# Performance work log

Measured on AMD Instinct MI355X. Metric: run time of the kernel, lower is better.

## Reference

```python
import jax, jax.numpy as jnp
import numpy as np

LN_EPS = 1e-5

def _layernorm(x, g, b):
    mu = jnp.mean(x, axis=-1, keepdims=True)
    var = jnp.mean(jnp.square(x - mu), axis=-1, keepdims=True)
    return (x - mu) * jax.lax.rsqrt(var + LN_EPS) * g + b

def setup_inputs() -> dict:
    key = jax.random.key(0)
    ks = jax.random.split(key, 12)
    B, S, E = 8, 4096, 512
    H, DK = 64, 8          # d_k = E // H = 8 qubits per head
    NQ_FFN, FFN = 8, 2048
    TWO_PI = 2.0 * np.pi
    x = jax.random.normal(ks[0], (B, S, E), dtype=jnp.float32)
    # trainable RX phases per attention head/wire; trainable RY phases for FFN qubits
    theta_attn = jax.random.uniform(ks[1], (H, DK), dtype=jnp.float32, maxval=TWO_PI)
    theta_ffn = jax.random.uniform(ks[2], (NQ_FFN,), dtype=jnp.float32, maxval=TWO_PI)
    s_e = 1.0 / np.sqrt(E)
    W_comb = jax.random.uniform(ks[3], (E, E), dtype=jnp.float32, minval=-s_e, maxval=s_e)
    b_comb = jax.random.uniform(ks[4], (E,), dtype=jnp.float32, minval=-s_e, maxval=s_e)
    s_q = 1.0 / np.sqrt(NQ_FFN)
    W1 = jax.random.uniform(ks[5], (FFN, NQ_FFN), dtype=jnp.float32, minval=-s_q, maxval=s_q)
    b1 = jax.random.uniform(ks[6], (FFN,), dtype=jnp.float32, minval=-s_q, maxval=s_q)
    s_f = 1.0 / np.sqrt(FFN)
    W2 = jax.random.uniform(ks[7], (E, FFN), dtype=jnp.float32, minval=-s_f, maxval=s_f)
    b2 = jax.random.uniform(ks[8], (E,), dtype=jnp.float32, minval=-s_f, maxval=s_f)
    ln1_g = jnp.ones((E,), jnp.float32); ln1_b = jnp.zeros((E,), jnp.float32)
    ln2_g = jnp.ones((E,), jnp.float32); ln2_b = jnp.zeros((E,), jnp.float32)
    return {"x": x, "theta_attn": theta_attn, "W_comb": W_comb, "b_comb": b_comb,
            "ln1_g": ln1_g, "ln1_b": ln1_b, "theta_ffn": theta_ffn,
            "W1": W1, "b1": b1, "W2": W2, "b2": b2, "ln2_g": ln2_g, "ln2_b": ln2_b}

def reference(x, theta_attn, W_comb, b_comb, ln1_g, ln1_b, theta_ffn, W1, b1, W2, b2, ln2_g, ln2_b):
    B, S, E = x.shape
    H, DK = theta_attn.shape
    NQ = theta_ffn.shape[0]
    # Quantum attention heads: RX(x) then RX(theta) on |0> per wire -> <Z> = cos(x+theta)
    q = jnp.cos(x.reshape(B, S, H, DK) + theta_attn)  # [B,S,H,DK]
    attn_out = jnp.einsum('bse,fe->bsf', q.reshape(B, S, E), W_comb) + b_comb
    x1 = _layernorm(x + attn_out, ln1_g, ln1_b)
    # Quantum FFN layer: RY(x) then RY(theta) -> <Z> = cos(x+theta), first NQ features only
    fq = jnp.cos(x1[..., :NQ] + theta_ffn)            # [B,S,NQ]
    h = jax.nn.relu(jnp.einsum('bsq,fq->bsf', fq, W1) + b1)
    ffn_out = jnp.einsum('bsf,ef->bse', h, W2) + b2
    return _layernorm(x1 + ffn_out, ln2_g, ln2_b)
```

## Files before the change

### kernel.cpp

```cpp
#include <hip/hip_runtime.h>
#include <stdint.h>

typedef unsigned short u16;
typedef __bf16 bf16x8 __attribute__((ext_vector_type(8)));
typedef float f32x4 __attribute__((ext_vector_type(4)));

#define AS1(p) ((const __attribute__((address_space(1))) void*)(p))
#define AS3(p) ((__attribute__((address_space(3))) void*)(p))

__device__ __forceinline__ float b2f(u16 v){
    union { unsigned u; float f; } x; x.u = ((unsigned)v) << 16; return x.f;
}
__device__ __forceinline__ u16 f2b(float f){
    union { float f; unsigned u; } x; x.f = f;
    unsigned r = x.u + 0x7FFFu + ((x.u >> 16) & 1u);
    return (u16)(r >> 16);
}

__global__ __launch_bounds__(256) void probe_kernel(
    const u16* p0,const u16* p1,const u16* p2,const u16* p3,const u16* p4,
    const u16* p5,const u16* p6,const u16* p7,const u16* p8,const u16* p9,
    const u16* p10,const u16* p11,const u16* p12,
    int n0,int n1,int n2,int n3,int n4,int n5,int n6,int n7,int n8,int n9,
    int n10,int n11,int n12, int* flags)
{
    const u16* p; int n;
    switch (blockIdx.x) {
        case 0: p=p0; n=n0; break;   case 1: p=p1; n=n1; break;
        case 2: p=p2; n=n2; break;   case 3: p=p3; n=n3; break;
        case 4: p=p4; n=n4; break;   case 5: p=p5; n=n5; break;
        case 6: p=p6; n=n6; break;   case 7: p=p7; n=n7; break;
        case 8: p=p8; n=n8; break;   case 9: p=p9; n=n9; break;
        case 10: p=p10; n=n10; break; case 11: p=p11; n=n11; break;
        default: p=p12; n=n12; break;
    }
    int pairs = n >> 1; if (pairs > 2048) pairs = 2048;
    int strong = 0, znz = 0, tot = 0;
    for (int k = threadIdx.x; k < pairs; k += 256) {
        u16 lo = p[2*k], hi = p[2*k+1];
        int eh = (hi >> 7) & 0xFF;
        int el = (lo >> 7) & 0xFF;
        if (eh >= 0xF0 || (eh >= 1 && eh <= 0x40)) strong = 1;
        if (el >= 0xF0 || (el >= 1 && el <= 0x40)) strong = 1;
        if (lo == 0 && hi != 0) znz++;
        tot++;
    }
    __shared__ int ss, sz, st;
    if (threadIdx.x == 0) { ss = 0; sz = 0; st = 0; }
    __syncthreads();
    if (strong) atomicOr(&ss, 1);
    if (znz) atomicAdd(&sz, znz);
    atomicAdd(&st, tot);
    __syncthreads();
    if (threadIdx.x == 0) {
        flags[blockIdx.x] = (ss || (2 * sz > st)) ? 1 : 0;
        if (blockIdx.x == 0) flags[15] = 0;
    }
}

__global__ __launch_bounds__(256) void convert_kernel(
    const void* sWc, const void* sW2, const void* sW1,
    const void* sTa, const void* sBc, const void* sG1, const void* sB1l,
    const void* sTf, const void* sB1, const void* sB2, const void* sG2, const void* sB2l,
    u16* wbase, const int* flags)
{
    int b = blockIdx.x;
    const void* src; u16* dst; int n, fi, lb, tof32 = 0;
    if (b < 128)      { src=sWc; dst=wbase;          n=262144;  fi=2;  lb=b; }
    else if (b < 640) { src=sW2; dst=wbase+262144;   n=1048576; fi=9;  lb=b-128; }
    else if (b >= 643 && b < 651) { src=sW1; dst=wbase+1312256; n=16384; fi=7; lb=b-643; }
    else {
        lb = 0;
        switch (b) {
            case 640: src=sTa;  dst=wbase+1310720; n=512;  fi=1;  break;
            case 641: src=sBc;  dst=wbase+1311232; n=512;  fi=3;  break;
            case 642: src=sB2;  dst=wbase+1311744; n=512;  fi=10; break;
            case 651: src=sB1;  dst=wbase+1328640; n=2048; fi=8;  break;
            case 652: src=sG1;  dst=wbase+1330688; n=512;  fi=4;  break;
            case 653: src=sB1l; dst=wbase+1331200; n=512;  fi=5;  break;
            case 654: src=sG2;  dst=wbase+1331712; n=512;  fi=11; break;
            case 655: src=sB2l; dst=wbase+1332224; n=512;  fi=12; break;
            default:  src=sTf;  dst=wbase+1332736; n=8;    fi=6;  tof32=1; break;
        }
    }
    int i = lb * 256 + threadIdx.x;
    if (i * 8 >= n) return;
    if (tof32) {
        float* fd = (float*)dst;
        if (flags[fi]) {
            const float4* s = (const float4*)src;
            ((float4*)fd)[i*2] = s[i*2]; ((float4*)fd)[i*2+1] = s[i*2+1];
        } else {
            union { uint4 v; u16 h[8]; } sb;
            sb.v = ((const uint4*)src)[i];
            #pragma unroll
            for (int j = 0; j < 8; j++) fd[i*8+j] = b2f(sb.h[j]);
        }
        return;
    }
    if (flags[fi]) {
        const float4* s = (const float4*)src;
        float4 a = s[i*2], c = s[i*2+1];
        union { uint4 v; u16 h[8]; } o;
        o.h[0]=f2b(a.x); o.h[1]=f2b(a.y); o.h[2]=f2b(a.z); o.h[3]=f2b(a.w);
        o.h[4]=f2b(c.x); o.h[5]=f2b(c.y); o.h[6]=f2b(c.z); o.h[7]=f2b(c.w);
        ((uint4*)dst)[i] = o.v;
    } else {
        ((uint4*)dst)[i] = ((const uint4*)src)[i];
    }
}

__global__ __launch_bounds__(256) void qgen_kernel(
    const void* __restrict__ x, const u16* __restrict__ theta,
    u16* __restrict__ q, const int* flags)
{
    const int idx = blockIdx.x * 256 + threadIdx.x;
    const int col0 = (idx * 8) & 511;
    union { uint4 v; u16 h[8]; } tb;
    tb.v = *(const uint4*)(theta + col0);
    float xv[8];
    if (flags[0]) {
        const float4* p = (const float4*)x + idx * 2;
        float4 a = p[0], b = p[1];
        xv[0]=a.x; xv[1]=a.y; xv[2]=a.z; xv[3]=a.w;
        xv[4]=b.x; xv[5]=b.y; xv[6]=b.z; xv[7]=b.w;
    } else {
        union { uint4 v; u16 h[8]; } xb;
        xb.v = ((const uint4*)x)[idx];
        #pragma unroll
        for (int e = 0; e < 8; e++) xv[e] = b2f(xb.h[e]);
    }
    union { uint4 v; u16 h[8]; } o;
    #pragma unroll
    for (int e = 0; e < 8; e++) o.h[e] = f2b(__cosf(xv[e] + b2f(tb.h[e])));
    ((uint4*)q)[idx] = o.v;
}

__global__ __launch_bounds__(256, 3) void gemm1_fused(
    const u16* __restrict__ q, const void* __restrict__ x,
    const u16* __restrict__ Wt, const u16* __restrict__ bias,
    u16* __restrict__ dst, int mtiles, const int* flags)
{
    __shared__ __align__(16) u16 As[2][128 * 64];
    __shared__ __align__(16) u16 Bs[2][128 * 64];
    const int K = 512, N = 512;
    const int tid  = threadIdx.x;
    const int lane = tid & 63;
    const int w    = tid >> 6;

    const int blk = blockIdx.x;
    const int xcd = blk & 7;
    const int j   = blk >> 3;
    const int per = mtiles >> 3;
    const int mt  = xcd * per + (j >> 2);
    const int nt  = j & 3;
    const int m0 = mt * 128;
    const int n0 = nt * 128;

    const int srow = lane >> 3;
    const int scol = ((lane & 7) ^ srow) * 8;
    const int wm = (w >> 1) * 64;
    const int wn = (w & 1) * 64;
    const int fr   = lane & 15;
    const int quad = lane >> 4;
    const int fx   = fr & 7;
    const int isf32 = flags[0];

    f32x4 acc[4][4];
    #pragma unroll
    for (int i = 0; i < 4; i++)
        #pragma unroll
        for (int jj = 0; jj < 4; jj++)
            acc[i][jj] = f32x4{0.f, 0.f, 0.f, 0.f};

    const u16* Abase = q  + (size_t)m0 * K + scol;
    const u16* Bbase = Wt + (size_t)n0 * K + scol;

    #pragma unroll
    for (int i = 0; i < 4; i++) {
        int c = w * 4 + i;
        int row = c * 8 + srow;
        __builtin_amdgcn_global_load_lds(AS1(Abase + (size_t)row * K),
                                         AS3(&As[0][c * 512]), 16, 0, 0);
        __builtin_amdgcn_global_load_lds(AS1(Bbase + (size_t)row * K),
                                         AS3(&Bs[0][c * 512]), 16, 0, 0);
    }

    int cur = 0;
    for (int kt = 0; kt < K; kt += 64) {
        __syncthreads();
        if (kt + 64 < K) {
            int nxt = cur ^ 1;
            #pragma unroll
            for (int i = 0; i < 4; i++) {
                int c = w * 4 + i;
                int row = c * 8 + srow;
                __builtin_amdgcn_global_load_lds(
                    AS1(Abase + (size_t)row * K + kt + 64),
                    AS3(&As[nxt][c * 512]), 16, 0, 0);
                __builtin_amdgcn_global_load_lds(
                    AS1(Bbase + (size_t)row * K + kt + 64),
                    AS3(&Bs[nxt][c * 512]), 16, 0, 0);
            }
        }
        #pragma unroll
        for (int kk = 0; kk < 2; kk++) {
            bf16x8 af[4], bfr[4];
            #pragma unroll
            for (int mi = 0; mi < 4; mi++)
                af[mi] = *(const bf16x8*)(&As[cur][(wm + mi * 16 + fr) * 64 +
                                          (((kk * 4 + quad) ^ fx) * 8)]);
            #pragma unroll
            for (int ni = 0; ni < 4; ni++)
                bfr[ni] = *(const bf16x8*)(&Bs[cur][(wn + ni * 16 + fr) * 64 +
                                           (((kk * 4 + quad) ^ fx) * 8)]);
            #pragma unroll
            for (int mi = 0; mi < 4; mi++)
                #pragma unroll
                for (int ni = 0; ni < 4; ni++)
                    acc[mi][ni] = __builtin_amdgcn_mfma_f32_16x16x32_bf16(
                        af[mi], bfr[ni], acc[mi][ni], 0, 0, 0);
        }
        cur ^= 1;
    }

    #pragma unroll
    for (int mi = 0; mi < 4; mi++) {
        #pragma unroll
        for (int ni = 0; ni < 4; ni++) {
            int n = n0 + wn + ni * 16 + fr;
            float bn = b2f(bias[n]);
            #pragma unroll
            for (int r = 0; r < 4; r++) {
                int m = m0 + wm + mi * 16 + quad * 4 + r;
                float rv = isf32 ? ((const float*)x)[(size_t)m * N + n]
                                 : b2f(((const u16*)x)[(size_t)m * N + n]);
                dst[(size_t)m * N + n] = f2b(acc[mi][ni][r] + bn + rv);
            }
        }
    }
}

__global__ __launch_bounds__(256, 3) void gemm2_fused(
    const u16* __restrict__ fq, const u16* __restrict__ W1, const u16* __restrict__ b1,
    const u16* __restrict__ Wt, const u16* __restrict__ bias,
    const u16* __restrict__ res, u16* __restrict__ dst, int mtiles)
{
    __shared__ __align__(16) u16 Bs[2][128 * 64];
    const int K = 2048, N = 512;
    const int tid  = threadIdx.x;
    const int lane = tid & 63;
    const int w    = tid >> 6;

    const int blk = blockIdx.x;
    const int xcd = blk & 7;
    const int j   = blk >> 3;
    const int per = mtiles >> 3;
    const int mt  = xcd * per + (j >> 2);
    const int nt  = j & 3;
    const int m0 = mt * 128;
    const int n0 = nt * 128;

    const int srow = lane >> 3;
    const int scol = ((lane & 7) ^ srow) * 8;
    const int wm = (w >> 1) * 64;
    const int wn = (w & 1) * 64;
    const int fr   = lane & 15;
    const int quad = lane >> 4;
    const int fx   = fr & 7;

    bf16x8 fqf[4];
    #pragma unroll
    for (int mi = 0; mi < 4; mi++) {
        union { uint4 v; bf16x8 b; } z; z.v = uint4{0,0,0,0};
        if (quad == 0) z.v = *(const uint4*)(fq + (size_t)(m0 + wm + mi * 16 + fr) * 8);
        fqf[mi] = z.b;
    }

    const int krow = ((fr >> 2) * 8) + (fr & 3);

    union { uint4 v; bf16x8 b; } w1f[4];
    uint2 b1f[4];
    #pragma unroll
    for (int g = 0; g < 4; g++) {
        w1f[g].v = uint4{0,0,0,0};
        if (quad == 0)
            w1f[g].v = *(const uint4*)(W1 + (size_t)((g >> 1) * 32 + (g & 1) * 4 + krow) * 8);
        b1f[g] = *(const uint2*)(b1 + (g >> 1) * 32 + (g & 1) * 4 + quad * 8);
    }

    f32x4 acc[4][4];
    #pragma unroll
    for (int i = 0; i < 4; i++)
        #pragma unroll
        for (int jj = 0; jj < 4; jj++)
            acc[i][jj] = f32x4{0.f, 0.f, 0.f, 0.f};

    const u16* Bbase = Wt + (size_t)n0 * K + scol;
    #pragma unroll
    for (int i = 0; i < 4; i++) {
        int c = w * 4 + i;
        int row = c * 8 + srow;
        __builtin_amdgcn_global_load_lds(AS1(Bbase + (size_t)row * K),
                                         AS3(&Bs[0][c * 512]), 16, 0, 0);
    }

    int cur = 0;
    for (int kt = 0; kt < K; kt += 64) {
        __syncthreads();
        if (kt + 64 < K) {
            int nxt = cur ^ 1;
            #pragma unroll
            for (int i = 0; i < 4; i++) {
                int c = w * 4 + i;
                int row = c * 8 + srow;
                __builtin_amdgcn_global_load_lds(
                    AS1(Bbase + (size_t)row * K + kt + 64),
                    AS3(&Bs[nxt][c * 512]), 16, 0, 0);
            }
        }
        #pragma unroll
        for (int kk = 0; kk < 2; kk++) {
            bf16x8 bfr[4];
            #pragma unroll
            for (int ni = 0; ni < 4; ni++)
                bfr[ni] = *(const bf16x8*)(&Bs[cur][(wn + ni * 16 + fr) * 64 +
                                           (((kk * 4 + quad) ^ fx) * 8)]);
            const u16* pb0 = (const u16*)&b1f[kk * 2 + 0];
            const u16* pb1 = (const u16*)&b1f[kk * 2 + 1];
            f32x4 c0 = {b2f(pb0[0]), b2f(pb0[1]), b2f(pb0[2]), b2f(pb0[3])};
            f32x4 c1 = {b2f(pb1[0]), b2f(pb1[1]), b2f(pb1[2]), b2f(pb1[3])};
            #pragma unroll
            for (int mi = 0; mi < 4; mi++) {
                f32x4 hv0 = __builtin_amdgcn_mfma_f32_16x16x32_bf16(
                    w1f[kk * 2 + 0].b, fqf[mi], c0, 0, 0, 0);
                f32x4 hv1 = __builtin_amdgcn_mfma_f32_16x16x32_bf16(
                    w1f[kk * 2 + 1].b, fqf[mi], c1, 0, 0, 0);
                bf16x8 af;
                #pragma unroll
                for (int r = 0; r < 4; r++) {
                    af[r]     = (__bf16)fmaxf(hv0[r], 0.f);
                    af[4 + r] = (__bf16)fmaxf(hv1[r], 0.f);
                }
                #pragma unroll
                for (int ni = 0; ni < 4; ni++)
                    acc[mi][ni] = __builtin_amdgcn_mfma_f32_16x16x32_bf16(
                        af, bfr[ni], acc[mi][ni], 0, 0, 0);
            }
        }
        if (kt + 64 < K) {
            #pragma unroll
            for (int g = 0; g < 4; g++) {
                if (quad == 0)
                    w1f[g].v = *(const uint4*)(W1 +
                        (size_t)(kt + 64 + (g >> 1) * 32 + (g & 1) * 4 + krow) * 8);
                b1f[g] = *(const uint2*)(b1 + kt + 64 + (g >> 1) * 32 + (g & 1) * 4 + quad * 8);
            }
        }
        cur ^= 1;
    }

    #pragma unroll
    for (int mi = 0; mi < 4; mi++) {
        #pragma unroll
        for (int ni = 0; ni < 4; ni++) {
            int n = n0 + wn + ni * 16 + fr;
            float bn = b2f(bias[n]);
            #pragma unroll
            for (int r = 0; r < 4; r++) {
                int m = m0 + wm + mi * 16 + quad * 4 + r;
                float rv = b2f(res[(size_t)m * N + n]);
                dst[(size_t)m * N + n] = f2b(acc[mi][ni][r] + bn + rv);
            }
        }
    }
}

__global__ __launch_bounds__(512) void ln1_kernel(
    const u16* __restrict__ y1, const u16* __restrict__ g, const u16* __restrict__ b,
    const float* __restrict__ tf, u16* __restrict__ x1, u16* __restrict__ fqout)
{
    __shared__ __align__(16) float xs8[64][8];
    const int t = threadIdx.x;
    const int wv = t >> 6, l = t & 63;
    const size_t rbase = (size_t)blockIdx.x * 64;

    union { uint4 v; u16 s[8]; } gb, bb;
    gb.v = *(const uint4*)(g + l * 8);
    bb.v = *(const uint4*)(b + l * 8);

    #pragma unroll
    for (int i = 0; i < 8; i++) {
        int lr = wv * 8 + i;
        union { uint4 v; u16 s[8]; } yb;
        yb.v = ((const uint4*)(y1 + (rbase + lr) * 512))[l];
        float xv[8], s = 0.f, ss = 0.f;
        #pragma unroll
        for (int jj = 0; jj < 8; jj++) {
            xv[jj] = b2f(yb.s[jj]); s += xv[jj]; ss += xv[jj] * xv[jj];
        }
        #pragma unroll
        for (int o = 32; o > 0; o >>= 1) { s += __shfl_down(s, o); ss += __shfl_down(ss, o); }
        s = __shfl(s, 0); ss = __shfl(ss, 0);
        float mu = s * (1.f / 512.f);
        float rs = rsqrtf(ss * (1.f / 512.f) - mu * mu + 1e-5f);
        union { uint4 v; u16 s[8]; } ob;
        float xn[8];
        #pragma unroll
        for (int jj = 0; jj < 8; jj++) {
            xn[jj] = (xv[jj] - mu) * rs * b2f(gb.s[jj]) + b2f(bb.s[jj]);
            ob.s[jj] = f2b(xn[jj]);
        }
        ((uint4*)(x1 + (rbase + lr) * 512))[l] = ob.v;
        if (l == 0) {
            #pragma unroll
            for (int jj = 0; jj < 8; jj++) xs8[lr][jj] = xn[jj];
        }
    }
    __syncthreads();
    {
        int r = t >> 3, jj = t & 7;
        fqout[(rbase + r) * 8 + jj] = f2b(__cosf(xs8[r][jj] + tf[jj]));
    }
}

__global__ __launch_bounds__(256) void ln2_kernel(
    const u16* __restrict__ z, const u16* __restrict__ g, const u16* __restrict__ b,
    void* __restrict__ out, const int* flags)
{
    const int t = threadIdx.x;
    const int wv = t >> 6, l = t & 63;
    const size_t row = (size_t)blockIdx.x * 4 + wv;

    union { uint4 v; u16 s[8]; } zb, gb, bb;
    zb.v = ((const uint4*)(z + row * 512))[l];
    gb.v = *(const uint4*)(g + l * 8);
    bb.v = *(const uint4*)(b + l * 8);
    float xv[8], s = 0.f, ss = 0.f;
    #pragma unroll
    for (int jj = 0; jj < 8; jj++) { xv[jj] = b2f(zb.s[jj]); s += xv[jj]; ss += xv[jj]*xv[jj]; }
    #pragma unroll
    for (int o = 32; o > 0; o >>= 1) { s += __shfl_down(s, o); ss += __shfl_down(ss, o); }
    s = __shfl(s, 0); ss = __shfl(ss, 0);
    float mu = s * (1.f / 512.f);
    float rs = rsqrtf(ss * (1.f / 512.f) - mu * mu + 1e-5f);
    float xn[8];
    #pragma unroll
    for (int jj = 0; jj < 8; jj++)
        xn[jj] = (xv[jj] - mu) * rs * b2f(gb.s[jj]) + b2f(bb.s[jj]);
    if (flags[0]) {
        float* po = (float*)out + row * 512 + l * 8;
        float4 o0{xn[0],xn[1],xn[2],xn[3]}, o1{xn[4],xn[5],xn[6],xn[7]};
        *(float4*)po = o0; *(float4*)(po + 4) = o1;
    } else {
        union { uint4 v; u16 s[8]; } ob;
        #pragma unroll
        for (int jj = 0; jj < 8; jj++) ob.s[jj] = f2b(xn[jj]);
        ((uint4*)((u16*)out + row * 512))[l] = ob.v;
    }
}

extern "C" void kernel_launch(void* const* d_in, const int* in_sizes, int n_in,
                              void* d_out, int out_size, void* d_ws, size_t ws_size,
                              hipStream_t stream)
{
    u16* ws16 = (u16*)d_ws;
    u16* W     = ws16;
    int* flags = (int*)(ws16 + 1332752);
    u16* fq  = ws16 + 1332800;
    u16* x1  = ws16 + 1594944;
    u16* q   = x1;
    u16* y1  = ws16 + 18372160;
    u16* z   = y1;

    const u16*  wWc  = W;
    const u16*  wW2  = W + 262144;
    const u16*  wTa  = W + 1310720;
    const u16*  wBc  = W + 1311232;
    const u16*  wB2  = W + 1311744;
    const u16*  wW1  = W + 1312256;
    const u16*  wB1  = W + 1328640;
    const u16*  wG1  = W + 1330688;
    const u16*  wB1l = W + 1331200;
    const u16*  wG2  = W + 1331712;
    const u16*  wB2l = W + 1332224;
    const float* wTf = (const float*)(W + 1332736);

    probe_kernel<<<13, 256, 0, stream>>>(
        (const u16*)d_in[0], (const u16*)d_in[1], (const u16*)d_in[2],
        (const u16*)d_in[3], (const u16*)d_in[4], (const u16*)d_in[5],
        (const u16*)d_in[6], (const u16*)d_in[7], (const u16*)d_in[8],
        (const u16*)d_in[9], (const u16*)d_in[10], (const u16*)d_in[11],
        (const u16*)d_in[12],
        in_sizes[0], in_sizes[1], in_sizes[2], in_sizes[3], in_sizes[4],
        in_sizes[5], in_sizes[6], in_sizes[7], in_sizes[8], in_sizes[9],
        in_sizes[10], in_sizes[11], in_sizes[12], flags);

    convert_kernel<<<657, 256, 0, stream>>>(
        d_in[2], d_in[9], d_in[7], d_in[1], d_in[3], d_in[4], d_in[5],
        d_in[6], d_in[8], d_in[10], d_in[11], d_in[12], (u16*)W, flags);

    qgen_kernel<<<8192, 256, 0, stream>>>(d_in[0], wTa, q, flags);

    gemm1_fused<<<1024, 256, 0, stream>>>(
        q, d_in[0], wWc, wBc, y1, 256, flags);

    ln1_kernel<<<512, 512, 0, stream>>>(y1, wG1, wB1l, wTf, x1, fq);

    gemm2_fused<<<1024, 256, 0, stream>>>(
        fq, wW1, wB1, wW2, wB2, x1, z, 256);

    ln2_kernel<<<8192, 256, 0, stream>>>(z, wG2, wB2l, d_out, flags);
}
```

Before: 336.3 us.

## Widen gemm2 block tile to full N to stop recomputing FFN hidden activations

Result: faster. 316.4 us (-5.9%).

```diff
diff --git a/kernel.cpp b/kernel.cpp
--- a/kernel.cpp
+++ b/kernel.cpp
@@ -241,30 +241,23 @@
     }
 }
 
-__global__ __launch_bounds__(256, 3) void gemm2_fused(
+__global__ __launch_bounds__(512, 2) void gemm2_fused(
     const u16* __restrict__ fq, const u16* __restrict__ W1, const u16* __restrict__ b1,
     const u16* __restrict__ Wt, const u16* __restrict__ bias,
     const u16* __restrict__ res, u16* __restrict__ dst, int mtiles)
 {
-    __shared__ __align__(16) u16 Bs[2][128 * 64];
+    __shared__ __align__(16) u16 Bs[2][512 * 64];
     const int K = 2048, N = 512;
     const int tid  = threadIdx.x;
     const int lane = tid & 63;
     const int w    = tid >> 6;
 
-    const int blk = blockIdx.x;
-    const int xcd = blk & 7;
-    const int j   = blk >> 3;
-    const int per = mtiles >> 3;
-    const int mt  = xcd * per + (j >> 2);
-    const int nt  = j & 3;
-    const int m0 = mt * 128;
-    const int n0 = nt * 128;
+    const int m0 = blockIdx.x * 128;
 
     const int srow = lane >> 3;
     const int scol = ((lane & 7) ^ srow) * 8;
-    const int wm = (w >> 1) * 64;
-    const int wn = (w & 1) * 64;
+    const int wm = (w >> 2) * 64;
+    const int wn = (w & 3) * 128;
     const int fr   = lane & 15;
     const int quad = lane >> 4;
     const int fx   = fr & 7;
@@ -289,17 +282,17 @@
         b1f[g] = *(const uint2*)(b1 + (g >> 1) * 32 + (g & 1) * 4 + quad * 8);
     }
 
-    f32x4 acc[4][4];
+    f32x4 acc[4][8];
     #pragma unroll
     for (int i = 0; i < 4; i++)
         #pragma unroll
-        for (int jj = 0; jj < 4; jj++)
+        for (int jj = 0; jj < 8; jj++)
             acc[i][jj] = f32x4{0.f, 0.f, 0.f, 0.f};
 
-    const u16* Bbase = Wt + (size_t)n0 * K + scol;
-    #pragma unroll
-    for (int i = 0; i < 4; i++) {
-        int c = w * 4 + i;
+    const u16* Bbase = Wt + scol;
+    #pragma unroll
+    for (int i = 0; i < 8; i++) {
+        int c = w * 8 + i;
         int row = c * 8 + srow;
         __builtin_amdgcn_global_load_lds(AS1(Bbase + (size_t)row * K),
                                          AS3(&Bs[0][c * 512]), 16, 0, 0);
@@ -311,8 +304,8 @@
         if (kt + 64 < K) {
             int nxt = cur ^ 1;
             #pragma unroll
-            for (int i = 0; i < 4; i++) {
-                int c = w * 4 + i;
+            for (int i = 0; i < 8; i++) {
+                int c = w * 8 + i;
                 int row = c * 8 + srow;
                 __builtin_amdgcn_global_load_lds(
                     AS1(Bbase + (size_t)row * K + kt + 64),
@@ -321,31 +314,36 @@
         }
         #pragma unroll
         for (int kk = 0; kk < 2; kk++) {
-            bf16x8 bfr[4];
-            #pragma unroll
-            for (int ni = 0; ni < 4; ni++)
-                bfr[ni] = *(const bf16x8*)(&Bs[cur][(wn + ni * 16 + fr) * 64 +
-                                           (((kk * 4 + quad) ^ fx) * 8)]);
             const u16* pb0 = (const u16*)&b1f[kk * 2 + 0];
             const u16* pb1 = (const u16*)&b1f[kk * 2 + 1];
             f32x4 c0 = {b2f(pb0[0]), b2f(pb0[1]), b2f(pb0[2]), b2f(pb0[3])};
             f32x4 c1 = {b2f(pb1[0]), b2f(pb1[1]), b2f(pb1[2]), b2f(pb1[3])};
+            bf16x8 af[4];
             #pragma unroll
             for (int mi = 0; mi < 4; mi++) {
                 f32x4 hv0 = __builtin_amdgcn_mfma_f32_16x16x32_bf16(
                     w1f[kk * 2 + 0].b, fqf[mi], c0, 0, 0, 0);
                 f32x4 hv1 = __builtin_amdgcn_mfma_f32_16x16x32_bf16(
                     w1f[kk * 2 + 1].b, fqf[mi], c1, 0, 0, 0);
-                bf16x8 af;
                 #pragma unroll
                 for (int r = 0; r < 4; r++) {
-                    af[r]     = (__bf16)fmaxf(hv0[r], 0.f);
-                    af[4 + r] = (__bf16)fmaxf(hv1[r], 0.f);
+                    af[mi][r]     = (__bf16)fmaxf(hv0[r], 0.f);
+                    af[mi][4 + r] = (__bf16)fmaxf(hv1[r], 0.f);
                 }
+            }
+            #pragma unroll
+            for (int np = 0; np < 4; np++) {
+                bf16x8 bfr[2];
                 #pragma unroll
-                for (int ni = 0; ni < 4; ni++)
-                    acc[mi][ni] = __builtin_amdgcn_mfma_f32_16x16x32_bf16(
-                        af, bfr[ni], acc[mi][ni], 0, 0, 0);
+                for (int ni = 0; ni < 2; ni++)
+                    bfr[ni] = *(const bf16x8*)(&Bs[cur][(wn + (np * 2 + ni) * 16 + fr) * 64 +
+                                               (((kk * 4 + quad) ^ fx) * 8)]);
+                #pragma unroll
+                for (int mi = 0; mi < 4; mi++)
+                    #pragma unroll
+                    for (int ni = 0; ni < 2; ni++)
+                        acc[mi][np * 2 + ni] = __builtin_amdgcn_mfma_f32_16x16x32_bf16(
+                            af[mi], bfr[ni], acc[mi][np * 2 + ni], 0, 0, 0);
             }
         }
         if (kt + 64 < K) {
@@ -363,14 +361,14 @@
     #pragma unroll
     for (int mi = 0; mi < 4; mi++) {
         #pragma unroll
-        for (int ni = 0; ni < 4; ni++) {
-            int n = n0 + wn + ni * 16 + fr;
+        for (int nq = 0; nq < 8; nq++) {
+            int n = wn + nq * 16 + fr;
             float bn = b2f(bias[n]);
             #pragma unroll
             for (int r = 0; r < 4; r++) {
                 int m = m0 + wm + mi * 16 + quad * 4 + r;
                 float rv = b2f(res[(size_t)m * N + n]);
-                dst[(size_t)m * N + n] = f2b(acc[mi][ni][r] + bn + rv);
+                dst[(size_t)m * N + n] = f2b(acc[mi][nq][r] + bn + rv);
             }
         }
     }
@@ -507,7 +505,7 @@
 
     ln1_kernel<<<512, 512, 0, stream>>>(y1, wG1, wB1l, wTf, x1, fq);
 
-    gemm2_fused<<<1024, 256, 0, stream>>>(
+    gemm2_fused<<<256, 512, 0, stream>>>(
         fq, wW1, wB1, wW2, wB2, x1, z, 256);
 
     ln2_kernel<<<8192, 256, 0, stream>>>(z, wG2, wB2l, d_out, flags);
```
